# Optimization experiments

Hardware: AMD Instinct MI355X
Metric: run time of the kernel (lower is better)

## Reference

```python
import jax, jax.numpy as jnp
import numpy as np

B, D, G, H = 65536, 512, 16, 128


def setup_inputs() -> dict:
    key = jax.random.key(0)
    ks = jax.random.split(key, 8)
    s = 1.0 / np.sqrt(D)
    sh = 1.0 / np.sqrt(H)
    return {
        "z": jax.random.normal(ks[0], (B, D), dtype=jnp.float32),
        "Wc": jax.random.uniform(ks[1], (D, G), jnp.float32, -s, s),
        "bc": jax.random.uniform(ks[2], (G,), jnp.float32, -s, s),
        "W1": jax.random.uniform(ks[3], (G, D, H), jnp.float32, -s, s),
        "b1": jax.random.uniform(ks[4], (G, H), jnp.float32, -s, s),
        "W2": jax.random.uniform(ks[5], (G, H), jnp.float32, -sh, sh),
        "b2": jax.random.uniform(ks[6], (G,), jnp.float32, -sh, sh),
    }


def reference(z, Wc, bc, W1, b1, W2, b2):
    # classifier head + softmax
    logits = z @ Wc + bc                                  # [B, G]
    p_g = jax.nn.softmax(logits, axis=1)                  # [B, G]
    # G experts fused as one batched GEMM: fc1 -> GELU -> fc2 (dropout = identity at eval)
    h = jax.nn.gelu(jnp.einsum('bd,gdh->bgh', z, W1) + b1, approximate=False)  # [B, G, H]
    y_all = jnp.einsum('bgh,gh->bg', h, W2) + b2          # [B, G]
    return logits, p_g, y_all
```

## Files before the change

### kernel.cpp

```cpp
#include <hip/hip_runtime.h>
#include <cstdint>
#include <cstddef>

typedef __bf16 bf16x8 __attribute__((ext_vector_type(8)));
typedef float f32x4 __attribute__((ext_vector_type(4)));
typedef unsigned int u32x4 __attribute__((ext_vector_type(4)));

__device__ __forceinline__ unsigned short f2bf(float f) {
  union { float f; unsigned int u; } v; v.f = f;
  return (unsigned short)((v.u + 0x8000u) >> 16);
}

__device__ __forceinline__ unsigned cvtpk(float a, float b) {
  unsigned r;
  asm("v_cvt_pk_bf16_f32 %0, %1, %2" : "=v"(r) : "v"(a), "v"(b));
  return r;
}

__device__ __forceinline__ float gelu_s(float x) {
  float x2 = x * x;
  float p = __builtin_fmaf(x2, -0.10294324f, -2.30220819f);
  float e = __builtin_amdgcn_exp2f(x * p);
  return x * __builtin_amdgcn_rcpf(1.0f + e);
}

#define GLOAD16(gsrc, ldst)                                                  \
  __builtin_amdgcn_global_load_lds(                                          \
      (const __attribute__((address_space(1))) unsigned int*)(gsrc),         \
      (__attribute__((address_space(3))) unsigned int*)(uintptr_t)(          \
          (char*)(ldst)),                                                    \
      16, 0, 0)

#define SWZ_FRAG(base, R, C8)                                                \
  (*(const bf16x8*)((base) + (((R) >> 5) * 4096) +                           \
                    ((((R)&31) * 8 + ((C8) ^ ((R)&7))) * 16)))

__device__ __forceinline__ void stage_A_f32(const float* __restrict__ ag,
                                            char* lds, int tid, int ko) {
  f32x4 a0[4], a1[4];
#pragma unroll
  for (int it = 0; it < 4; ++it) {
    const float* p = ag + it * 32 * 512 + ko;
    a0[it] = *(const f32x4*)(p);
    a1[it] = *(const f32x4*)(p + 4);
  }
#pragma unroll
  for (int it = 0; it < 4; ++it) {
    u32x4 v;
    v[0] = cvtpk(a0[it][0], a0[it][1]);
    v[1] = cvtpk(a0[it][2], a0[it][3]);
    v[2] = cvtpk(a1[it][0], a1[it][1]);
    v[3] = cvtpk(a1[it][2], a1[it][3]);
    *(u32x4*)(lds + it * 4096 + tid * 16) = v;
  }
}

__device__ __forceinline__ void expert_tile(
    int e, int mbase, const float* __restrict__ z,
    const unsigned short* __restrict__ w1t, const float* __restrict__ b1,
    const float* __restrict__ w2, const float* __restrict__ b2,
    float* __restrict__ out, char* lds, int tid, int wq, int l15, int l4,
    int c8s) {
  char* ldsB = lds + 16384;
  const float* ag = z + (size_t)(mbase + (tid >> 3)) * 512 + c8s;
  const unsigned short* bg = w1t + e * 65536 + (tid >> 3) * 512 + c8s;
  const int wr = wq >> 1;
  const int wc = wq & 1;
  f32x4 acc[4][4] = {};
  for (int kt = 0; kt < 8; ++kt) {
    const int ko = kt * 64;
#pragma unroll
    for (int it = 0; it < 4; ++it)
      GLOAD16(bg + it * 32 * 512 + ko, ldsB + it * 4096 + tid * 16);
    stage_A_f32(ag, lds, tid, ko);
    __syncthreads();
#pragma unroll
    for (int ks = 0; ks < 2; ++ks) {
      bf16x8 af[4];
#pragma unroll
      for (int rt = 0; rt < 4; ++rt)
        af[rt] = SWZ_FRAG(lds, wr * 64 + rt * 16 + l15, ks * 4 + l4);
#pragma unroll
      for (int ct = 0; ct < 4; ++ct) {
        bf16x8 bfv = SWZ_FRAG(ldsB, wc * 64 + ct * 16 + l15, ks * 4 + l4);
#pragma unroll
        for (int rt = 0; rt < 4; ++rt)
          acc[rt][ct] = __builtin_amdgcn_mfma_f32_16x16x32_bf16(
              af[rt], bfv, acc[rt][ct], 0, 0, 0);
      }
    }
    __syncthreads();
  }
  float b1v[4], w2v[4];
#pragma unroll
  for (int ct = 0; ct < 4; ++ct) {
    int n = wc * 64 + ct * 16 + l15;
    b1v[ct] = b1[e * 128 + n];
    w2v[ct] = w2[e * 128 + n];
  }
  float* ylds = (float*)(lds + 32768);
#pragma unroll
  for (int rt = 0; rt < 4; ++rt) {
#pragma unroll
    for (int i = 0; i < 4; ++i) {
      float s = 0.0f;
#pragma unroll
      for (int ct = 0; ct < 4; ++ct)
        s += gelu_s(acc[rt][ct][i] + b1v[ct]) * w2v[ct];
#pragma unroll
      for (int off = 1; off < 16; off <<= 1) s += __shfl_xor(s, off, 16);
      if (l15 == 0) ylds[wq * 64 + rt * 16 + l4 * 4 + i] = s;
    }
  }
  __syncthreads();
  if (tid < 128) {
    int rl = tid & 63, half = tid >> 6;
    float y = ylds[half * 128 + rl] + ylds[half * 128 + 64 + rl] + b2[e];
    out[(size_t)2097152 + (size_t)(mbase + half * 64 + rl) * 16 + e] = y;
  }
}

__device__ __forceinline__ void logits_tile(
    int mbase, const float* __restrict__ z,
    const unsigned short* __restrict__ wct, const float* __restrict__ bc,
    float* __restrict__ out, char* lds, int tid, int wq, int l15, int l4,
    int c8s) {
  const float* ag = z + (size_t)(mbase + (tid >> 3)) * 512 + c8s;
  const unsigned short* wb = wct + l15 * 512 + l4 * 8;
  f32x4 acc2[2] = {};
  for (int kt = 0; kt < 8; ++kt) {
    const int ko = kt * 64;
    stage_A_f32(ag, lds, tid, ko);
    bf16x8 bfr0 = *(const bf16x8*)(wb + ko);
    bf16x8 bfr1 = *(const bf16x8*)(wb + ko + 32);
    __syncthreads();
#pragma unroll
    for (int rt = 0; rt < 2; ++rt) {
      bf16x8 a0 = SWZ_FRAG(lds, wq * 32 + rt * 16 + l15, l4);
      acc2[rt] =
          __builtin_amdgcn_mfma_f32_16x16x32_bf16(a0, bfr0, acc2[rt], 0, 0, 0);
      bf16x8 a1 = SWZ_FRAG(lds, wq * 32 + rt * 16 + l15, 4 + l4);
      acc2[rt] =
          __builtin_amdgcn_mfma_f32_16x16x32_bf16(a1, bfr1, acc2[rt], 0, 0, 0);
    }
    __syncthreads();
  }
  float bcv = bc[l15];
#pragma unroll
  for (int rt = 0; rt < 2; ++rt) {
#pragma unroll
    for (int i = 0; i < 4; ++i) {
      int row = wq * 32 + rt * 16 + l4 * 4 + i;
      float lg = acc2[rt][i] + bcv;
      float mx = lg;
#pragma unroll
      for (int off = 1; off < 16; off <<= 1)
        mx = fmaxf(mx, __shfl_xor(mx, off, 16));
      float ex = __expf(lg - mx);
      float sm = ex;
#pragma unroll
      for (int off = 1; off < 16; off <<= 1) sm += __shfl_xor(sm, off, 16);
      size_t ro = (size_t)(mbase + row) * 16 + l15;
      out[ro] = lg;
      out[1048576 + ro] = ex / sm;
    }
  }
}

__global__ __launch_bounds__(256) void k_convert(
    const float* __restrict__ W1, const float* __restrict__ Wc,
    unsigned short* __restrict__ w1t, unsigned short* __restrict__ wct) {
  int bid = blockIdx.x;
  int tid = threadIdx.x;
  if (bid < 1024) {
    __shared__ float tile[32][33];
    int gg = bid >> 6;
    int t = bid & 63;
    int d0 = (t >> 2) * 32;
    int h0 = (t & 3) * 32;
    int tx = tid & 31, ty = tid >> 5;
#pragma unroll
    for (int r = 0; r < 4; ++r)
      tile[r * 8 + ty][tx] = W1[(gg << 16) + (d0 + r * 8 + ty) * 128 + h0 + tx];
    __syncthreads();
#pragma unroll
    for (int r = 0; r < 4; ++r)
      w1t[(gg << 16) + (h0 + r * 8 + ty) * 512 + d0 + tx] =
          f2bf(tile[tx][r * 8 + ty]);
  } else {
#pragma unroll
    for (int j = 0; j < 32; ++j) {
      int i = j * 256 + tid;
      wct[(i & 15) * 512 + (i >> 4)] = f2bf(Wc[i]);
    }
  }
}

__global__ __launch_bounds__(256, 4) void k_main(
    const float* __restrict__ z, const unsigned short* __restrict__ w1t,
    const unsigned short* __restrict__ wct, const float* __restrict__ bc,
    const float* __restrict__ b1, const float* __restrict__ w2,
    const float* __restrict__ b2, float* __restrict__ out) {
  __shared__ alignas(16) char lds[33792];
  const int tid = threadIdx.x;
  const int wq = tid >> 6;
  const int l15 = tid & 15;
  const int l4 = (tid >> 4) & 3;
  const int c8s = (((tid & 7) ^ ((tid >> 3) & 7))) * 8;
  const int xcd = blockIdx.x & 7;
  const int t = blockIdx.x >> 3;
  const int pl = t / 17;
  const int r = t - pl * 17;
  const int mbase = (xcd * 64 + pl) * 128;
  if (r == 0)
    logits_tile(mbase, z, wct, bc, out, lds, tid, wq, l15, l4, c8s);
  else
    expert_tile(r - 1, mbase, z, w1t, b1, w2, b2, out, lds, tid, wq, l15, l4,
                c8s);
}

extern "C" void kernel_launch(void* const* d_in, const int* in_sizes, int n_in,
                              void* d_out, int out_size, void* d_ws,
                              size_t ws_size, hipStream_t stream) {
  const float* z = (const float*)d_in[0];
  const float* Wc = (const float*)d_in[1];
  const float* bc = (const float*)d_in[2];
  const float* W1 = (const float*)d_in[3];
  const float* b1 = (const float*)d_in[4];
  const float* W2 = (const float*)d_in[5];
  const float* b2 = (const float*)d_in[6];
  float* out = (float*)d_out;

  unsigned short* w1t = (unsigned short*)d_ws;
  unsigned short* wct = w1t + (size_t)16 * 128 * 512;

  k_convert<<<1024 + 1, 256, 0, stream>>>(W1, Wc, w1t, wct);
  k_main<<<8 * 1088, 256, 0, stream>>>(z, w1t, wct, bc, b1, W2, b2, out);
}
```

Baseline: 351.7 us.

## Process two experts per 512-thread block to share staged z tile

Each workgroup grows to 512 threads (8 waves) and computes two experts at once. Waves 0-3 handle one expert and waves 4-7 the other, both reading the same bf16 A tile of z staged once in LDS. This halves the number of times each z tile is loaded from global memory and converted from fp32, and the grid shrinks from 17 to 9 tiles per row block. The logits tile is remapped to 8 waves of 16 rows each. In exchange LDS per block grows to about 50 KB and the larger block may reduce occupancy or scheduling flexibility.

```diff
diff --git a/kernel.cpp b/kernel.cpp
--- a/kernel.cpp
+++ b/kernel.cpp
@@ -35,44 +35,49 @@
   (*(const bf16x8*)((base) + (((R) >> 5) * 4096) +                           \
                     ((((R)&31) * 8 + ((C8) ^ ((R)&7))) * 16)))
 
-__device__ __forceinline__ void stage_A_f32(const float* __restrict__ ag,
+__device__ __forceinline__ void stage_A_512(const float* __restrict__ ag,
                                             char* lds, int tid, int ko) {
-  f32x4 a0[4], a1[4];
-#pragma unroll
-  for (int it = 0; it < 4; ++it) {
-    const float* p = ag + it * 32 * 512 + ko;
+  f32x4 a0[2], a1[2];
+#pragma unroll
+  for (int it = 0; it < 2; ++it) {
+    const float* p = ag + it * 64 * 512 + ko;
     a0[it] = *(const f32x4*)(p);
     a1[it] = *(const f32x4*)(p + 4);
   }
 #pragma unroll
-  for (int it = 0; it < 4; ++it) {
+  for (int it = 0; it < 2; ++it) {
     u32x4 v;
     v[0] = cvtpk(a0[it][0], a0[it][1]);
     v[1] = cvtpk(a0[it][2], a0[it][3]);
     v[2] = cvtpk(a1[it][0], a1[it][1]);
     v[3] = cvtpk(a1[it][2], a1[it][3]);
-    *(u32x4*)(lds + it * 4096 + tid * 16) = v;
-  }
-}
-
-__device__ __forceinline__ void expert_tile(
-    int e, int mbase, const float* __restrict__ z,
+    *(u32x4*)(lds + it * 8192 + tid * 16) = v;
+  }
+}
+
+__device__ __forceinline__ void expert_pair_tile(
+    int e0, int mbase, const float* __restrict__ z,
     const unsigned short* __restrict__ w1t, const float* __restrict__ b1,
     const float* __restrict__ w2, const float* __restrict__ b2,
     float* __restrict__ out, char* lds, int tid, int wq, int l15, int l4,
     int c8s) {
   char* ldsB = lds + 16384;
   const float* ag = z + (size_t)(mbase + (tid >> 3)) * 512 + c8s;
-  const unsigned short* bg = w1t + e * 65536 + (tid >> 3) * 512 + c8s;
-  const int wr = wq >> 1;
+  const unsigned short* bg = w1t + e0 * 65536 + (tid >> 3) * 512 + c8s;
+  const int esub = wq >> 2;
+  const int wr = (wq >> 1) & 1;
   const int wc = wq & 1;
+  char* ldsBe = ldsB + esub * 16384;
   f32x4 acc[4][4] = {};
   for (int kt = 0; kt < 8; ++kt) {
     const int ko = kt * 64;
 #pragma unroll
-    for (int it = 0; it < 4; ++it)
-      GLOAD16(bg + it * 32 * 512 + ko, ldsB + it * 4096 + tid * 16);
-    stage_A_f32(ag, lds, tid, ko);
+    for (int sub = 0; sub < 2; ++sub)
+#pragma unroll
+      for (int it = 0; it < 2; ++it)
+        GLOAD16(bg + sub * 65536 + it * 64 * 512 + ko,
+                ldsB + sub * 16384 + it * 8192 + tid * 16);
+    stage_A_512(ag, lds, tid, ko);
     __syncthreads();
 #pragma unroll
     for (int ks = 0; ks < 2; ++ks) {
@@ -82,7 +87,7 @@
         af[rt] = SWZ_FRAG(lds, wr * 64 + rt * 16 + l15, ks * 4 + l4);
 #pragma unroll
       for (int ct = 0; ct < 4; ++ct) {
-        bf16x8 bfv = SWZ_FRAG(ldsB, wc * 64 + ct * 16 + l15, ks * 4 + l4);
+        bf16x8 bfv = SWZ_FRAG(ldsBe, wc * 64 + ct * 16 + l15, ks * 4 + l4);
 #pragma unroll
         for (int rt = 0; rt < 4; ++rt)
           acc[rt][ct] = __builtin_amdgcn_mfma_f32_16x16x32_bf16(
@@ -91,6 +96,7 @@
     }
     __syncthreads();
   }
+  const int e = e0 + esub;
   float b1v[4], w2v[4];
 #pragma unroll
   for (int ct = 0; ct < 4; ++ct) {
@@ -98,7 +104,7 @@
     b1v[ct] = b1[e * 128 + n];
     w2v[ct] = w2[e * 128 + n];
   }
-  float* ylds = (float*)(lds + 32768);
+  float* ylds = (float*)(lds + 49152);
 #pragma unroll
   for (int rt = 0; rt < 4; ++rt) {
 #pragma unroll
@@ -113,10 +119,14 @@
     }
   }
   __syncthreads();
-  if (tid < 128) {
-    int rl = tid & 63, half = tid >> 6;
-    float y = ylds[half * 128 + rl] + ylds[half * 128 + 64 + rl] + b2[e];
-    out[(size_t)2097152 + (size_t)(mbase + half * 64 + rl) * 16 + e] = y;
+  if (tid < 256) {
+    int rl = tid & 63;
+    int half = (tid >> 6) & 1;
+    int es = tid >> 7;
+    float y = ylds[(es * 4 + half * 2) * 64 + rl] +
+              ylds[(es * 4 + half * 2 + 1) * 64 + rl] + b2[e0 + es];
+    out[(size_t)2097152 + (size_t)(mbase + half * 64 + rl) * 16 + e0 + es] =
+        y;
   }
 }
 
@@ -127,43 +137,35 @@
     int c8s) {
   const float* ag = z + (size_t)(mbase + (tid >> 3)) * 512 + c8s;
   const unsigned short* wb = wct + l15 * 512 + l4 * 8;
-  f32x4 acc2[2] = {};
+  f32x4 acc2 = {};
   for (int kt = 0; kt < 8; ++kt) {
     const int ko = kt * 64;
-    stage_A_f32(ag, lds, tid, ko);
+    stage_A_512(ag, lds, tid, ko);
     bf16x8 bfr0 = *(const bf16x8*)(wb + ko);
     bf16x8 bfr1 = *(const bf16x8*)(wb + ko + 32);
     __syncthreads();
-#pragma unroll
-    for (int rt = 0; rt < 2; ++rt) {
-      bf16x8 a0 = SWZ_FRAG(lds, wq * 32 + rt * 16 + l15, l4);
-      acc2[rt] =
-          __builtin_amdgcn_mfma_f32_16x16x32_bf16(a0, bfr0, acc2[rt], 0, 0, 0);
-      bf16x8 a1 = SWZ_FRAG(lds, wq * 32 + rt * 16 + l15, 4 + l4);
-      acc2[rt] =
-          __builtin_amdgcn_mfma_f32_16x16x32_bf16(a1, bfr1, acc2[rt], 0, 0, 0);
-    }
+    bf16x8 a0 = SWZ_FRAG(lds, wq * 16 + l15, l4);
+    acc2 = __builtin_amdgcn_mfma_f32_16x16x32_bf16(a0, bfr0, acc2, 0, 0, 0);
+    bf16x8 a1 = SWZ_FRAG(lds, wq * 16 + l15, 4 + l4);
+    acc2 = __builtin_amdgcn_mfma_f32_16x16x32_bf16(a1, bfr1, acc2, 0, 0, 0);
     __syncthreads();
   }
   float bcv = bc[l15];
 #pragma unroll
-  for (int rt = 0; rt < 2; ++rt) {
-#pragma unroll
-    for (int i = 0; i < 4; ++i) {
-      int row = wq * 32 + rt * 16 + l4 * 4 + i;
-      float lg = acc2[rt][i] + bcv;
-      float mx = lg;
-#pragma unroll
-      for (int off = 1; off < 16; off <<= 1)
-        mx = fmaxf(mx, __shfl_xor(mx, off, 16));
-      float ex = __expf(lg - mx);
-      float sm = ex;
-#pragma unroll
-      for (int off = 1; off < 16; off <<= 1) sm += __shfl_xor(sm, off, 16);
-      size_t ro = (size_t)(mbase + row) * 16 + l15;
-      out[ro] = lg;
-      out[1048576 + ro] = ex / sm;
-    }
+  for (int i = 0; i < 4; ++i) {
+    int row = wq * 16 + l4 * 4 + i;
+    float lg = acc2[i] + bcv;
+    float mx = lg;
+#pragma unroll
+    for (int off = 1; off < 16; off <<= 1)
+      mx = fmaxf(mx, __shfl_xor(mx, off, 16));
+    float ex = __expf(lg - mx);
+    float sm = ex;
+#pragma unroll
+    for (int off = 1; off < 16; off <<= 1) sm += __shfl_xor(sm, off, 16);
+    size_t ro = (size_t)(mbase + row) * 16 + l15;
+    out[ro] = lg;
+    out[1048576 + ro] = ex / sm;
   }
 }
 
@@ -196,12 +198,12 @@
   }
 }
 
-__global__ __launch_bounds__(256, 4) void k_main(
+__global__ __launch_bounds__(512, 6) void k_main(
     const float* __restrict__ z, const unsigned short* __restrict__ w1t,
     const unsigned short* __restrict__ wct, const float* __restrict__ bc,
     const float* __restrict__ b1, const float* __restrict__ w2,
     const float* __restrict__ b2, float* __restrict__ out) {
-  __shared__ alignas(16) char lds[33792];
+  __shared__ alignas(16) char lds[16384 + 32768 + 2048];
   const int tid = threadIdx.x;
   const int wq = tid >> 6;
   const int l15 = tid & 15;
@@ -209,14 +211,14 @@
   const int c8s = (((tid & 7) ^ ((tid >> 3) & 7))) * 8;
   const int xcd = blockIdx.x & 7;
   const int t = blockIdx.x >> 3;
-  const int pl = t / 17;
-  const int r = t - pl * 17;
+  const int pl = t / 9;
+  const int r = t - pl * 9;
   const int mbase = (xcd * 64 + pl) * 128;
   if (r == 0)
     logits_tile(mbase, z, wct, bc, out, lds, tid, wq, l15, l4, c8s);
   else
-    expert_tile(r - 1, mbase, z, w1t, b1, w2, b2, out, lds, tid, wq, l15, l4,
-                c8s);
+    expert_pair_tile((r - 1) * 2, mbase, z, w1t, b1, w2, b2, out, lds, tid,
+                     wq, l15, l4, c8s);
 }
 
 extern "C" void kernel_launch(void* const* d_in, const int* in_sizes, int n_in,
@@ -235,5 +237,5 @@
   unsigned short* wct = w1t + (size_t)16 * 128 * 512;
 
   k_convert<<<1024 + 1, 256, 0, stream>>>(W1, Wc, w1t, wct);
-  k_main<<<8 * 1088, 256, 0, stream>>>(z, w1t, wct, bc, b1, W2, b2, out);
-}
+  k_main<<<8 * 576, 512, 0, stream>>>(z, w1t, wct, bc, b1, W2, b2, out);
+}
```

New measurement: 1.222 ms. 247% more time.
